# Optimization experiments

Measured on AMD Instinct MI355X. Metric: run time of the kernel, lower is better.

## Reference

```python
import jax, jax.numpy as jnp
import numpy as np

N, IN_F, OUT_F = 10000, 512, 64
ALPHA = 0.2       # leaky relu slope
THRESHOLD = 0.01  # hub threshold
NEG_INF = -9.0e15


def setup_inputs() -> dict:
    key = jax.random.key(0)
    k_h, k_adj, k_hub, k_W, k_as, k_ad = jax.random.split(key, 6)
    h = jax.random.normal(k_h, (N, IN_F), dtype=jnp.float32)
    adj = jax.random.randint(k_adj, (N, N), 0, 2, dtype=jnp.int32)
    hub_mask = jax.random.uniform(k_hub, (N,), dtype=jnp.float32)
    # xavier-uniform-ish params (gain 1.414)
    lim_W = 1.414 * np.sqrt(6.0 / (IN_F + OUT_F))
    W = jax.random.uniform(k_W, (IN_F, OUT_F), minval=-lim_W, maxval=lim_W, dtype=jnp.float32)
    lim_a = 1.414 * np.sqrt(6.0 / (OUT_F + 1))
    a_src = jax.random.uniform(k_as, (OUT_F, 1), minval=-lim_a, maxval=lim_a, dtype=jnp.float32)
    a_dst = jax.random.uniform(k_ad, (OUT_F, 1), minval=-lim_a, maxval=lim_a, dtype=jnp.float32)
    return {"h": h, "W": W, "a_src": a_src, "a_dst": a_dst, "hub_mask": hub_mask, "adj": adj}


def reference(h, W, a_src, a_dst, hub_mask, adj):
    Wh = h @ W                                  # [N, F_out]
    e_src = Wh @ a_src                          # [N, 1]
    e_dst = Wh @ a_dst                          # [N, 1]
    e = jax.nn.leaky_relu(e_src + e_dst.T, negative_slope=ALPHA)  # [N, N]
    scores = jnp.where(adj > 0, e, jnp.float32(NEG_INF))
    attention = jax.nn.softmax(scores, axis=1)  # row-wise softmax over neighbors
    attention = jax.nn.relu(attention - hub_mask * THRESHOLD)  # hub threshold prune
    # dropout omitted (inference mode / p applied as no-op for deterministic reference)
    h_prime = attention @ Wh                    # [N, F_out]
    return jax.nn.elu(h_prime)                  # concat=True branch
```

## Files before the change

### kernel.cpp

```cpp
#include <hip/hip_runtime.h>
#include <math.h>

#define N_NODES 10000
#define IN_FEAT 512
#define OUT_FEAT 64
#define LRELU_ALPHA 0.2f
#define HUB_THRESH 0.01f
#define BITS_WORDS 320
#define CAND_CAP 1024
#define PREF_SLACK 0.9394131f

#define WH_OFF   0
#define ESRC_OFF 640000
#define EDST_OFF 650000
#define T_OFF    660000
#define F1_OFF   670000
#define F2_OFF   680000
#define AL_OFF   690000
#define BE_OFF   700000

__global__ __launch_bounds__(256) void k1_gemm(
    const float* __restrict__ h, const float* __restrict__ W,
    const float* __restrict__ a_src, const float* __restrict__ a_dst,
    float* __restrict__ ws)
{
    const int bx = blockIdx.x, tid = threadIdx.x;
    __shared__ __align__(16) float Ws[64 * 64];
    __shared__ __align__(16) float Hs[16 * 68];
    const int row_l = tid >> 4;
    const int q     = tid & 15;
    const int c4    = q * 4;
    const int row   = bx * 16 + row_l;
    float4 acc = make_float4(0.f, 0.f, 0.f, 0.f);

    for (int k0 = 0; k0 < IN_FEAT; k0 += 64) {
        const float4* __restrict__ W4 = (const float4*)(W + (size_t)k0 * 64);
        float4* Ws4 = (float4*)Ws;
        #pragma unroll
        for (int t = 0; t < 4; ++t) Ws4[tid + t * 256] = W4[tid + t * 256];
        *(float4*)&Hs[row_l * 68 + c4] =
            *(const float4*)&h[(size_t)row * IN_FEAT + k0 + c4];
        __syncthreads();
        #pragma unroll
        for (int k4 = 0; k4 < 16; ++k4) {
            float4 hv = *(const float4*)&Hs[row_l * 68 + k4 * 4];
            float4 w0 = *(const float4*)&Ws[(k4 * 4 + 0) * 64 + c4];
            float4 w1 = *(const float4*)&Ws[(k4 * 4 + 1) * 64 + c4];
            float4 w2 = *(const float4*)&Ws[(k4 * 4 + 2) * 64 + c4];
            float4 w3 = *(const float4*)&Ws[(k4 * 4 + 3) * 64 + c4];
            acc.x += hv.x * w0.x + hv.y * w1.x + hv.z * w2.x + hv.w * w3.x;
            acc.y += hv.x * w0.y + hv.y * w1.y + hv.z * w2.y + hv.w * w3.y;
            acc.z += hv.x * w0.z + hv.y * w1.z + hv.z * w2.z + hv.w * w3.z;
            acc.w += hv.x * w0.w + hv.y * w1.w + hv.z * w2.w + hv.w * w3.w;
        }
        __syncthreads();
    }

    *(float4*)&ws[WH_OFF + (size_t)row * 64 + c4] = acc;
    const float4 as4 = *(const float4*)&a_src[c4];
    const float4 ad4 = *(const float4*)&a_dst[c4];
    float s1 = acc.x * as4.x + acc.y * as4.y + acc.z * as4.z + acc.w * as4.w;
    float s2 = acc.x * ad4.x + acc.y * ad4.y + acc.z * ad4.z + acc.w * ad4.w;
    #pragma unroll
    for (int m = 1; m <= 8; m <<= 1) {
        s1 += __shfl_xor(s1, m, 64);
        s2 += __shfl_xor(s2, m, 64);
    }
    if (q == 0) {
        ws[ESRC_OFF + row] = s1;
        ws[EDST_OFF + row] = s2;
    }
}

__global__ __launch_bounds__(256) void k1b_prep(
    const float* __restrict__ hub, float* __restrict__ ws)
{
    const int j = blockIdx.x * 256 + threadIdx.x;
    if (j < N_NODES) {
        float ed = ws[EDST_OFF + j];
        float F1 = __expf(ed);
        float F2 = __expf(0.2f * ed);
        float t  = hub[j] * HUB_THRESH;
        ws[F1_OFF + j] = F1;
        ws[F2_OFF + j] = F2;
        ws[T_OFF  + j] = t;
        ws[AL_OFF + j] = F1 / t;
        ws[BE_OFF + j] = F2 / t;
    }
}

__global__ __launch_bounds__(256) void k2_fused(
    const int* __restrict__ adj, const float* __restrict__ ws,
    float* __restrict__ out)
{
    const int b = blockIdx.x, tid = threadIdx.x;
    const int lane = tid & 63, w = tid >> 6;
    const int i0 = 2 * b, i1 = 2 * b + 1;
    __shared__ unsigned bits[2][BITS_WORDS];
    __shared__ float partA[2][4];
    __shared__ int2  cand[2][CAND_CAP];
    __shared__ int   cnt[2];
    __shared__ float oaccL[2][64];

    const float esrc0 = ws[ESRC_OFF + i0];
    const float esrc1 = ws[ESRC_OFF + i1];
    const float E1_0 = __expf(esrc0), E2_0 = __expf(0.2f * esrc0);
    const float E1_1 = __expf(esrc1), E2_1 = __expf(0.2f * esrc1);
    const float R0 = E2_0 / E1_0, R1 = E2_1 / E1_1;
    const int4*   __restrict__ arow0 = (const int4*)(adj + (size_t)i0 * N_NODES);
    const int4*   __restrict__ arow1 = (const int4*)(adj + (size_t)i1 * N_NODES);
    const float4* __restrict__ F14   = (const float4*)(ws + F1_OFF);
    const float4* __restrict__ F24   = (const float4*)(ws + F2_OFF);
    float acc0 = 0.f, acc1 = 0.f;

    if (tid < 2) cnt[tid] = 0;
    if (tid < 128) ((float*)oaccL)[tid] = 0.f;

#define PA_BODY(IT, A0v, A1v, F1v, F2v)                                      \
    {                                                                        \
        float v0, v1;                                                        \
        unsigned long long B0, B1, B2, B3, B4, B5, B6, B7;                   \
        v0 = fmaxf((F1v).x, R0 * (F2v).x);                                   \
        v1 = fmaxf((F1v).x, R1 * (F2v).x);                                   \
        if ((A0v).x > 0) acc0 += v0;                                         \
        if ((A1v).x > 0) acc1 += v1;                                         \
        B0 = __ballot((A0v).x > 0);                                          \
        B4 = __ballot((A1v).x > 0);                                          \
        v0 = fmaxf((F1v).y, R0 * (F2v).y);                                   \
        v1 = fmaxf((F1v).y, R1 * (F2v).y);                                   \
        if ((A0v).y > 0) acc0 += v0;                                         \
        if ((A1v).y > 0) acc1 += v1;                                         \
        B1 = __ballot((A0v).y > 0);                                          \
        B5 = __ballot((A1v).y > 0);                                          \
        v0 = fmaxf((F1v).z, R0 * (F2v).z);                                   \
        v1 = fmaxf((F1v).z, R1 * (F2v).z);                                   \
        if ((A0v).z > 0) acc0 += v0;                                         \
        if ((A1v).z > 0) acc1 += v1;                                         \
        B2 = __ballot((A0v).z > 0);                                          \
        B6 = __ballot((A1v).z > 0);                                          \
        v0 = fmaxf((F1v).w, R0 * (F2v).w);                                   \
        v1 = fmaxf((F1v).w, R1 * (F2v).w);                                   \
        if ((A0v).w > 0) acc0 += v0;                                         \
        if ((A1v).w > 0) acc1 += v1;                                         \
        B3 = __ballot((A0v).w > 0);                                          \
        B7 = __ballot((A1v).w > 0);                                          \
        if (lane < 8) {                                                      \
            \
            unsigned long long v =                                           \
                (lane & 4) ? ((lane & 2) ? ((lane & 1) ? B7 : B6)            \
                                         : ((lane & 1) ? B5 : B4))           \
                           : ((lane & 2) ? ((lane & 1) ? B3 : B2)            \
                                         : ((lane & 1) ? B1 : B0));          \
            *((unsigned long long*)&bits[lane >> 2][0] +                     \
              ((IT) * 16 + w * 4 + (lane & 3))) = v;                         \
        }                                                                    \
    }

    #pragma unroll 3
    for (int it = 0; it < 9; ++it) {
        int4   a0 = arow0[it * 256 + tid];
        int4   a1 = arow1[it * 256 + tid];
        float4 f1 = F14[it * 256 + tid];
        float4 f2 = F24[it * 256 + tid];
        PA_BODY(it, a0, a1, f1, f2)
    }
    {
        const int j0t = 9216 + tid * 4;
        int4   a0 = make_int4(0, 0, 0, 0), a1 = make_int4(0, 0, 0, 0);
        float4 f1 = make_float4(0.f, 0.f, 0.f, 0.f), f2 = f1;
        if (j0t < N_NODES) {
            a0 = arow0[9 * 256 + tid];
            a1 = arow1[9 * 256 + tid];
            f1 = F14[9 * 256 + tid];
            f2 = F24[9 * 256 + tid];
        }
        PA_BODY(9, a0, a1, f1, f2)
    }
#undef PA_BODY

    #pragma unroll
    for (int m = 32; m; m >>= 1) {
        acc0 += __shfl_xor(acc0, m, 64);
        acc1 += __shfl_xor(acc1, m, 64);
    }
    if (lane == 0) { partA[0][w] = acc0; partA[1][w] = acc1; }
    __syncthreads();
    const float l0 = E1_0 * (partA[0][0] + partA[0][1] + partA[0][2] + partA[0][3]);
    const float l1 = E1_1 * (partA[1][0] + partA[1][1] + partA[1][2] + partA[1][3]);

    const bool empty0 = (l0 == 0.0f), empty1 = (l1 == 0.0f);
    const float cl0 = empty0 ? 0.0f : logf(l0);
    const float cl1 = empty1 ? 0.0f : logf(l1);
    const float A0 = PREF_SLACK * l0 / E1_0, B0v = PREF_SLACK * l0 / E2_0;
    const float A1 = PREF_SLACK * l1 / E1_1, B1v = PREF_SLACK * l1 / E2_1;
    const float invN = 1.0f / (float)N_NODES;
    const float* __restrict__ tarr = ws + T_OFF;
    const float* __restrict__ edst = ws + EDST_OFF;
    const float* __restrict__ alp  = ws + AL_OFF;
    const float* __restrict__ bet  = ws + BE_OFF;
    const float* __restrict__ Wh   = ws + WH_OFF;
    float oacc0 = 0.f, oacc1 = 0.f;
    const unsigned rm0 = empty0 ? 0u : 0xffffffffu;
    const unsigned rm1 = empty1 ? 0u : 0xffffffffu;
    const unsigned lb = lane & 31;

#define PB_TEST(WROW, Athr, Bthr, ESRC, CL, R, ALc, BEc, JC)                 \
    if ((((WROW) >> lb) & 1u) && ((ALc) > (Athr) || (BEc) > (Bthr))) {       \
        float ed = edst[JC];                                                 \
        float s = (ESRC) + ed;                                               \
        float e = fmaxf(s, LRELU_ALPHA * s);                                 \
        float p = __expf(e - (CL));                          \
        float wgt = p - tarr[JC];                            \
        if (wgt > 0.0f) {                                                    \
            int k = atomicAdd(&cnt[R], 1);                                   \
            if (k < CAND_CAP) {                                              \
                cand[R][k] = make_int2((JC), __float_as_int(wgt));           \
            } else {      \
                const float* whp = Wh + (size_t)(JC) * 64;                   \
                for (int cc = 0; cc < 64; ++cc)                              \
                    atomicAdd(&oaccL[R][cc], wgt * whp[cc]);                 \
            }                                                                \
        }                                                                    \
    }

    #pragma unroll 2
    for (int it = 0; it < 10; ++it) {
        const int j0 = it * 1024 + tid * 4;
        if (j0 < N_NODES) {
            const int wb = it * 32 + w * 8 + (lane >> 5);
            const unsigned w00 = bits[0][wb + 0] & rm0;
            const unsigned w01 = bits[0][wb + 2] & rm0;
            const unsigned w02 = bits[0][wb + 4] & rm0;
            const unsigned w03 = bits[0][wb + 6] & rm0;
            const unsigned w10 = bits[1][wb + 0] & rm1;
            const unsigned w11 = bits[1][wb + 2] & rm1;
            const unsigned w12 = bits[1][wb + 4] & rm1;
            const unsigned w13 = bits[1][wb + 6] & rm1;
            if (((w00 | w01 | w02 | w03 | w10 | w11 | w12 | w13) >> lb) & 1u) {
                float4 al4 = *(const float4*)(alp + j0);
                float4 be4 = *(const float4*)(bet + j0);
                PB_TEST(w00, A0, B0v, esrc0, cl0, 0, al4.x, be4.x, j0 + 0)
                PB_TEST(w10, A1, B1v, esrc1, cl1, 1, al4.x, be4.x, j0 + 0)
                PB_TEST(w01, A0, B0v, esrc0, cl0, 0, al4.y, be4.y, j0 + 1)
                PB_TEST(w11, A1, B1v, esrc1, cl1, 1, al4.y, be4.y, j0 + 1)
                PB_TEST(w02, A0, B0v, esrc0, cl0, 0, al4.z, be4.z, j0 + 2)
                PB_TEST(w12, A1, B1v, esrc1, cl1, 1, al4.z, be4.z, j0 + 2)
                PB_TEST(w03, A0, B0v, esrc0, cl0, 0, al4.w, be4.w, j0 + 3)
                PB_TEST(w13, A1, B1v, esrc1, cl1, 1, al4.w, be4.w, j0 + 3)
            }
        }
        if ((empty0 | empty1) && j0 < N_NODES) {
            float4 t4 = *(const float4*)(tarr + j0);
            #pragma unroll
            for (int c = 0; c < 4; ++c) {
                float tv = (c == 0) ? t4.x : (c == 1) ? t4.y : (c == 2) ? t4.z : t4.w;
                float wv = invN - tv;
                if (wv > 0.0f) {
                    #pragma unroll
                    for (int r = 0; r < 2; ++r) {
                        if (r == 0 ? empty0 : empty1) {
                            int k = atomicAdd(&cnt[r], 1);
                            if (k < CAND_CAP) {
                                cand[r][k] = make_int2(j0 + c, __float_as_int(wv));
                            } else {
                                const float* whp = Wh + (size_t)(j0 + c) * 64;
                                for (int cc = 0; cc < 64; ++cc)
                                    atomicAdd(&oaccL[r][cc], wv * whp[cc]);
                            }
                        }
                    }
                }
            }
        }
    }
#undef PB_TEST

    __syncthreads();
    const int M0 = min(cnt[0], CAND_CAP), M1 = min(cnt[1], CAND_CAP);

    int c0 = w;
    for (; c0 + 12 < M0; c0 += 16) {
        int2 cd0 = cand[0][c0];
        int2 cd1 = cand[0][c0 + 4];
        int2 cd2 = cand[0][c0 + 8];
        int2 cd3 = cand[0][c0 + 12];
        float v0 = Wh[(size_t)cd0.x * 64 + lane];
        float v1 = Wh[(size_t)cd1.x * 64 + lane];
        float v2 = Wh[(size_t)cd2.x * 64 + lane];
        float v3 = Wh[(size_t)cd3.x * 64 + lane];
        oacc0 += __int_as_float(cd0.y) * v0;
        oacc0 += __int_as_float(cd1.y) * v1;
        oacc0 += __int_as_float(cd2.y) * v2;
        oacc0 += __int_as_float(cd3.y) * v3;
    }
    for (; c0 < M0; c0 += 4) {
        int2 cd = cand[0][c0];
        oacc0 += __int_as_float(cd.y) * Wh[(size_t)cd.x * 64 + lane];
    }
    int c1 = w;
    for (; c1 + 12 < M1; c1 += 16) {
        int2 cd0 = cand[1][c1];
        int2 cd1 = cand[1][c1 + 4];
        int2 cd2 = cand[1][c1 + 8];
        int2 cd3 = cand[1][c1 + 12];
        float v0 = Wh[(size_t)cd0.x * 64 + lane];
        float v1 = Wh[(size_t)cd1.x * 64 + lane];
        float v2 = Wh[(size_t)cd2.x * 64 + lane];
        float v3 = Wh[(size_t)cd3.x * 64 + lane];
        oacc1 += __int_as_float(cd0.y) * v0;
        oacc1 += __int_as_float(cd1.y) * v1;
        oacc1 += __int_as_float(cd2.y) * v2;
        oacc1 += __int_as_float(cd3.y) * v3;
    }
    for (; c1 < M1; c1 += 4) {
        int2 cd = cand[1][c1];
        oacc1 += __int_as_float(cd.y) * Wh[(size_t)cd.x * 64 + lane];
    }

    float* partB = (float*)bits;
    partB[tid]       = oacc0;
    partB[256 + tid] = oacc1;
    __syncthreads();
    if (w < 2) {
        const float* pb = partB + w * 256;
        float tot = pb[lane] + pb[64 + lane] + pb[128 + lane] + pb[192 + lane]
                  + oaccL[w][lane];
        out[(size_t)(i0 + w) * 64 + lane] = tot > 0.0f ? tot : expm1f(tot);
    }
}

extern "C" void kernel_launch(void* const* d_in, const int* in_sizes, int n_in,
                              void* d_out, int out_size, void* d_ws, size_t ws_size,
                              hipStream_t stream)
{
    const float* h     = (const float*)d_in[0];
    const float* W     = (const float*)d_in[1];
    const float* a_src = (const float*)d_in[2];
    const float* a_dst = (const float*)d_in[3];
    const float* hub   = (const float*)d_in[4];
    const int*   adj   = (const int*)d_in[5];
    float* ws  = (float*)d_ws;
    float* out = (float*)d_out;

    k1_gemm<<<625, 256, 0, stream>>>(h, W, a_src, a_dst, ws);
    k1b_prep<<<40, 256, 0, stream>>>(hub, ws);
    k2_fused<<<N_NODES / 2, 256, 0, stream>>>(adj, ws, out);
}
```

Before: 592.0 us.

## Split GEMM K-loop across wavefronts with register tiling and fuse prep kernel

The projection GEMM is restructured so each wavefront handles a quarter of the K slice and each thread keeps a 4x4 register tile, which raises reuse of loaded W and h values. The four K-partial results are then reduced through shared memory. The separate per-node prep kernel (exp of e_dst, hub threshold, ratios) is folded into the GEMM epilogue, removing one launch. This adds a shared-memory reduction pass and an extra barrier, and since the large adjacency kernel dominates total time the overall effect is likely small.

```diff
diff --git a/kernel.cpp b/kernel.cpp
--- a/kernel.cpp
+++ b/kernel.cpp
@@ -22,70 +22,103 @@
 __global__ __launch_bounds__(256) void k1_gemm(
     const float* __restrict__ h, const float* __restrict__ W,
     const float* __restrict__ a_src, const float* __restrict__ a_dst,
-    float* __restrict__ ws)
+    const float* __restrict__ hub, float* __restrict__ ws)
 {
     const int bx = blockIdx.x, tid = threadIdx.x;
-    __shared__ __align__(16) float Ws[64 * 64];
-    __shared__ __align__(16) float Hs[16 * 68];
-    const int row_l = tid >> 4;
-    const int q     = tid & 15;
-    const int c4    = q * 4;
-    const int row   = bx * 16 + row_l;
-    float4 acc = make_float4(0.f, 0.f, 0.f, 0.f);
+    __shared__ __align__(16) float smem[5184];
+    float* Ws = smem;
+    float* Hs = smem + 4096;
+    const int ks = tid >> 6;
+    const int slot = tid & 63;
+    const int rg = slot >> 4;
+    const int cq = slot & 15;
+    const int rowBase = bx * 16;
+    float4 acc0 = make_float4(0.f,0.f,0.f,0.f);
+    float4 acc1 = make_float4(0.f,0.f,0.f,0.f);
+    float4 acc2 = make_float4(0.f,0.f,0.f,0.f);
+    float4 acc3 = make_float4(0.f,0.f,0.f,0.f);
 
     for (int k0 = 0; k0 < IN_FEAT; k0 += 64) {
         const float4* __restrict__ W4 = (const float4*)(W + (size_t)k0 * 64);
-        float4* Ws4 = (float4*)Ws;
         #pragma unroll
-        for (int t = 0; t < 4; ++t) Ws4[tid + t * 256] = W4[tid + t * 256];
-        *(float4*)&Hs[row_l * 68 + c4] =
-            *(const float4*)&h[(size_t)row * IN_FEAT + k0 + c4];
+        for (int t = 0; t < 4; ++t) ((float4*)Ws)[tid + t * 256] = W4[tid + t * 256];
+        {
+            const int hr = tid >> 4, kq = tid & 15;
+            *(float4*)&Hs[hr * 68 + kq * 4] =
+                *(const float4*)&h[(size_t)(rowBase + hr) * IN_FEAT + k0 + kq * 4];
+        }
         __syncthreads();
         #pragma unroll
-        for (int k4 = 0; k4 < 16; ++k4) {
-            float4 hv = *(const float4*)&Hs[row_l * 68 + k4 * 4];
-            float4 w0 = *(const float4*)&Ws[(k4 * 4 + 0) * 64 + c4];
-            float4 w1 = *(const float4*)&Ws[(k4 * 4 + 1) * 64 + c4];
-            float4 w2 = *(const float4*)&Ws[(k4 * 4 + 2) * 64 + c4];
-            float4 w3 = *(const float4*)&Ws[(k4 * 4 + 3) * 64 + c4];
-            acc.x += hv.x * w0.x + hv.y * w1.x + hv.z * w2.x + hv.w * w3.x;
-            acc.y += hv.x * w0.y + hv.y * w1.y + hv.z * w2.y + hv.w * w3.y;
-            acc.z += hv.x * w0.z + hv.y * w1.z + hv.z * w2.z + hv.w * w3.z;
-            acc.w += hv.x * w0.w + hv.y * w1.w + hv.z * w2.w + hv.w * w3.w;
+        for (int s = 0; s < 4; ++s) {
+            const int kl = ks * 16 + s * 4;
+            float4 h0 = *(const float4*)&Hs[(rg * 4 + 0) * 68 + kl];
+            float4 h1 = *(const float4*)&Hs[(rg * 4 + 1) * 68 + kl];
+            float4 h2 = *(const float4*)&Hs[(rg * 4 + 2) * 68 + kl];
+            float4 h3 = *(const float4*)&Hs[(rg * 4 + 3) * 68 + kl];
+            float4 w0 = *(const float4*)&Ws[(kl + 0) * 64 + cq * 4];
+            float4 w1 = *(const float4*)&Ws[(kl + 1) * 64 + cq * 4];
+            float4 w2 = *(const float4*)&Ws[(kl + 2) * 64 + cq * 4];
+            float4 w3 = *(const float4*)&Ws[(kl + 3) * 64 + cq * 4];
+            acc0.x += h0.x*w0.x + h0.y*w1.x + h0.z*w2.x + h0.w*w3.x;
+            acc0.y += h0.x*w0.y + h0.y*w1.y + h0.z*w2.y + h0.w*w3.y;
+            acc0.z += h0.x*w0.z + h0.y*w1.z + h0.z*w2.z + h0.w*w3.z;
+            acc0.w += h0.x*w0.w + h0.y*w1.w + h0.z*w2.w + h0.w*w3.w;
+            acc1.x += h1.x*w0.x + h1.y*w1.x + h1.z*w2.x + h1.w*w3.x;
+            acc1.y += h1.x*w0.y + h1.y*w1.y + h1.z*w2.y + h1.w*w3.y;
+            acc1.z += h1.x*w0.z + h1.y*w1.z + h1.z*w2.z + h1.w*w3.z;
+            acc1.w += h1.x*w0.w + h1.y*w1.w + h1.z*w2.w + h1.w*w3.w;
+            acc2.x += h2.x*w0.x + h2.y*w1.x + h2.z*w2.x + h2.w*w3.x;
+            acc2.y += h2.x*w0.y + h2.y*w1.y + h2.z*w2.y + h2.w*w3.y;
+            acc2.z += h2.x*w0.z + h2.y*w1.z + h2.z*w2.z + h2.w*w3.z;
+            acc2.w += h2.x*w0.w + h2.y*w1.w + h2.z*w2.w + h2.w*w3.w;
+            acc3.x += h3.x*w0.x + h3.y*w1.x + h3.z*w2.x + h3.w*w3.x;
+            acc3.y += h3.x*w0.y + h3.y*w1.y + h3.z*w2.y + h3.w*w3.y;
+            acc3.z += h3.x*w0.z + h3.y*w1.z + h3.z*w2.z + h3.w*w3.z;
+            acc3.w += h3.x*w0.w + h3.y*w1.w + h3.z*w2.w + h3.w*w3.w;
         }
         __syncthreads();
     }
 
-    *(float4*)&ws[WH_OFF + (size_t)row * 64 + c4] = acc;
-    const float4 as4 = *(const float4*)&a_src[c4];
-    const float4 ad4 = *(const float4*)&a_dst[c4];
-    float s1 = acc.x * as4.x + acc.y * as4.y + acc.z * as4.z + acc.w * as4.w;
-    float s2 = acc.x * ad4.x + acc.y * ad4.y + acc.z * ad4.z + acc.w * ad4.w;
-    #pragma unroll
-    for (int m = 1; m <= 8; m <<= 1) {
-        s1 += __shfl_xor(s1, m, 64);
-        s2 += __shfl_xor(s2, m, 64);
-    }
-    if (q == 0) {
-        ws[ESRC_OFF + row] = s1;
-        ws[EDST_OFF + row] = s2;
-    }
-}
-
-__global__ __launch_bounds__(256) void k1b_prep(
-    const float* __restrict__ hub, float* __restrict__ ws)
-{
-    const int j = blockIdx.x * 256 + threadIdx.x;
-    if (j < N_NODES) {
-        float ed = ws[EDST_OFF + j];
-        float F1 = __expf(ed);
-        float F2 = __expf(0.2f * ed);
-        float t  = hub[j] * HUB_THRESH;
-        ws[F1_OFF + j] = F1;
-        ws[F2_OFF + j] = F2;
-        ws[T_OFF  + j] = t;
-        ws[AL_OFF + j] = F1 / t;
-        ws[BE_OFF + j] = F2 / t;
+    float* red = smem;
+    *(float4*)&red[ks * 1088 + (rg * 4 + 0) * 68 + cq * 4] = acc0;
+    *(float4*)&red[ks * 1088 + (rg * 4 + 1) * 68 + cq * 4] = acc1;
+    *(float4*)&red[ks * 1088 + (rg * 4 + 2) * 68 + cq * 4] = acc2;
+    *(float4*)&red[ks * 1088 + (rg * 4 + 3) * 68 + cq * 4] = acc3;
+    __syncthreads();
+
+    {
+        const int r = tid >> 4, c = tid & 15;
+        float4 a0 = *(const float4*)&red[0 * 1088 + r * 68 + c * 4];
+        float4 a1 = *(const float4*)&red[1 * 1088 + r * 68 + c * 4];
+        float4 a2 = *(const float4*)&red[2 * 1088 + r * 68 + c * 4];
+        float4 a3 = *(const float4*)&red[3 * 1088 + r * 68 + c * 4];
+        float4 tot = make_float4(a0.x + a1.x + a2.x + a3.x,
+                                 a0.y + a1.y + a2.y + a3.y,
+                                 a0.z + a1.z + a2.z + a3.z,
+                                 a0.w + a1.w + a2.w + a3.w);
+        const int row = rowBase + r;
+        *(float4*)&ws[WH_OFF + (size_t)row * 64 + c * 4] = tot;
+        const float4 as4 = *(const float4*)&a_src[c * 4];
+        const float4 ad4 = *(const float4*)&a_dst[c * 4];
+        float s1 = tot.x * as4.x + tot.y * as4.y + tot.z * as4.z + tot.w * as4.w;
+        float s2 = tot.x * ad4.x + tot.y * ad4.y + tot.z * ad4.z + tot.w * ad4.w;
+        #pragma unroll
+        for (int m = 1; m <= 8; m <<= 1) {
+            s1 += __shfl_xor(s1, m, 64);
+            s2 += __shfl_xor(s2, m, 64);
+        }
+        if (c == 0) {
+            ws[ESRC_OFF + row] = s1;
+            ws[EDST_OFF + row] = s2;
+            float F1 = __expf(s2);
+            float F2 = __expf(0.2f * s2);
+            float t  = hub[row] * HUB_THRESH;
+            ws[T_OFF  + row] = t;
+            ws[F1_OFF + row] = F1;
+            ws[F2_OFF + row] = F2;
+            ws[AL_OFF + row] = F1 / t;
+            ws[BE_OFF + row] = F2 / t;
+        }
     }
 }
 
@@ -342,7 +375,6 @@
     float* ws  = (float*)d_ws;
     float* out = (float*)d_out;
 
-    k1_gemm<<<625, 256, 0, stream>>>(h, W, a_src, a_dst, ws);
-    k1b_prep<<<40, 256, 0, stream>>>(hub, ws);
+    k1_gemm<<<625, 256, 0, stream>>>(h, W, a_src, a_dst, hub, ws);
     k2_fused<<<N_NODES / 2, 256, 0, stream>>>(adj, ws, out);
 }
```

Result: no change. 585.4 us (-1.1%).
